# Kernel tuning notes

Hardware: AMD Instinct MI355X
Metric: run time of the kernel (lower is better)

## Reference

```python
import jax, jax.numpy as jnp
import numpy as np

D_MODEL = 768
D_INNER = 1536
D_STATE = 16
D_CONV = 4
DT_RANK = 48
BATCH = 1
SEQ = 2048


def setup_inputs() -> dict:
    key = jax.random.key(0)
    ks = jax.random.split(key, 8)
    s = 0.02
    x = jax.random.normal(ks[0], (BATCH, SEQ, D_MODEL), dtype=jnp.float32)
    W_in = jax.random.normal(ks[1], (2 * D_INNER, D_MODEL), dtype=jnp.float32) * s
    conv_w = jax.random.normal(ks[2], (D_INNER, 1, D_CONV), dtype=jnp.float32) * s
    conv_b = jnp.zeros((D_INNER,), dtype=jnp.float32)
    W_x = jax.random.normal(ks[3], (DT_RANK + 2 * D_STATE, D_INNER), dtype=jnp.float32) * s
    W_dt = jax.random.normal(ks[4], (D_INNER, DT_RANK), dtype=jnp.float32) * s
    b_dt = jax.random.normal(ks[5], (D_INNER,), dtype=jnp.float32) * s
    # A = arange(1, d_state+1) broadcast over d_inner; parameter is log(A)
    A_log = jnp.log(jnp.broadcast_to(jnp.arange(1, D_STATE + 1, dtype=jnp.float32), (D_INNER, D_STATE)))
    D_param = jnp.ones((D_INNER,), dtype=jnp.float32)
    W_out = jax.random.normal(ks[6], (D_MODEL, D_INNER), dtype=jnp.float32) * s
    return {"x": x, "W_in": W_in, "conv_w": conv_w, "conv_b": conv_b, "W_x": W_x,
            "W_dt": W_dt, "b_dt": b_dt, "A_log": A_log, "D_param": D_param, "W_out": W_out}


def _mamba_forward(x, W_in, conv_w, conv_b, W_x, W_dt, b_dt, A_log, D_param, W_out):
    B, L, _ = x.shape
    # in_proj and split into conv branch and gate
    xz = x @ W_in.T                              # [B, L, 2*d_inner]
    xb, z = jnp.split(xz, 2, axis=-1)
    # causal depthwise conv1d (padding=d_conv-1 then trim == left pad d_conv-1)
    xc = jnp.transpose(xb, (0, 2, 1))            # [B, d_inner, L]
    xc = jax.lax.conv_general_dilated(
        xc, conv_w, window_strides=(1,), padding=[(D_CONV - 1, 0)],
        feature_group_count=D_INNER, dimension_numbers=("NCH", "OIH", "NCH"))
    xc = xc + conv_b[None, :, None]
    xb = jax.nn.silu(jnp.transpose(xc, (0, 2, 1)))  # [B, L, d_inner]
    # input-dependent dt, B, C
    xdbl = xb @ W_x.T                            # [B, L, dt_rank + 2*d_state]
    dt = xdbl[..., :DT_RANK]
    Bm = xdbl[..., DT_RANK:DT_RANK + D_STATE]
    Cm = xdbl[..., DT_RANK + D_STATE:]
    dt = jax.nn.softplus(dt @ W_dt.T + b_dt)     # [B, L, d_inner]
    # discretize
    A = -jnp.exp(A_log)                          # [d_inner, d_state]
    dA = jnp.exp(jnp.einsum("bld,dn->bldn", dt, A))          # [B, L, d_inner, d_state]
    dBx = dt[..., None] * Bm[:, :, None, :] * xb[..., None]   # dB * x, [B, L, d_inner, d_state]
    # sequential scan: h[t] = dA[t]*h[t-1] + dBx[t]; y[t] = <h[t], C[t]>
    def step(h, inp):
        dA_t, dBx_t, C_t = inp
        h = dA_t * h + dBx_t                     # [B, d_inner, d_state]
        y_t = jnp.einsum("bdn,bn->bd", h, C_t)
        return h, y_t
    h0 = jnp.zeros((B, D_INNER, D_STATE), dtype=x.dtype)
    _, ys = jax.lax.scan(step, h0, (jnp.moveaxis(dA, 1, 0), jnp.moveaxis(dBx, 1, 0), jnp.moveaxis(Cm, 1, 0)))
    y = jnp.moveaxis(ys, 0, 1) + xb * D_param    # [B, L, d_inner]
    # gate and output projection
    y = y * jax.nn.silu(z)
    return y @ W_out.T                           # [B, L, d_model]


def reference(x, W_in, conv_w, conv_b, W_x, W_dt, b_dt, A_log, D_param, W_out):
    return _mamba_forward(x, W_in, conv_w, conv_b, W_x, W_dt, b_dt, A_log, D_param, W_out)
```

## Files before the change

kernel.cpp:

```cpp
#include <hip/hip_runtime.h>
#include <hip/hip_bf16.h>

#define D_MODEL 768
#define D_INNER 1536
#define D_STATE 16
#define DT_RANK 48
#define SEQ 2048
#define NC 32
#define LC (SEQ / NC)
#define DN (D_INNER * D_STATE)
#define KS 8
#define KCH (D_INNER / KS)

typedef float f32x4 __attribute__((ext_vector_type(4)));
typedef short bf16x8 __attribute__((ext_vector_type(8)));

typedef const __attribute__((address_space(1))) unsigned int* gas_u32;
typedef __attribute__((address_space(3))) unsigned int* las_u32;

__device__ __forceinline__ void gload16(const void* g, void* l) {
  __builtin_amdgcn_global_load_lds((gas_u32)g, (las_u32)l, 16, 0, 0);
}

__device__ __forceinline__ float dpp_radd16(float v) {
  int x;
  x = __builtin_amdgcn_update_dpp(0, __float_as_int(v), 0xB1, 0xF, 0xF, true);
  v += __int_as_float(x);
  x = __builtin_amdgcn_update_dpp(0, __float_as_int(v), 0x4E, 0xF, 0xF, true);
  v += __int_as_float(x);
  x = __builtin_amdgcn_update_dpp(0, __float_as_int(v), 0x141, 0xF, 0xF, true);
  v += __int_as_float(x);
  x = __builtin_amdgcn_update_dpp(0, __float_as_int(v), 0x140, 0xF, 0xF, true);
  v += __int_as_float(x);
  return v;
}

__device__ __forceinline__ ushort f2bf_bits(float f) {
  uint u = __float_as_uint(f);
  u += 0x7FFFu + ((u >> 16) & 1u);
  return (ushort)(u >> 16);
}
__device__ __forceinline__ float bf_bits2f(ushort b) {
  return __uint_as_float(((uint)b) << 16);
}

__device__ __forceinline__ void split_vec4(const float* __restrict__ src,
                                           ushort* __restrict__ hi,
                                           ushort* __restrict__ lo, int idx) {
  const float4 v = ((const float4*)src)[idx];
  const float f[4] = {v.x, v.y, v.z, v.w};
  ushort4 h, l;
  ushort* hp = (ushort*)&h;
  ushort* lp = (ushort*)&l;
#pragma unroll
  for (int j = 0; j < 4; ++j) {
    const ushort hb = f2bf_bits(f[j]);
    hp[j] = hb;
    lp[j] = f2bf_bits(f[j] - bf_bits2f(hb));
  }
  ((ushort4*)hi)[idx] = h;
  ((ushort4*)lo)[idx] = l;
}

__global__ __launch_bounds__(256) void split3_bf16_kernel(
    const float* __restrict__ s0, ushort* __restrict__ h0, ushort* __restrict__ l0, int n0v,
    const float* __restrict__ s1, ushort* __restrict__ h1, ushort* __restrict__ l1, int n1v,
    const float* __restrict__ s2, ushort* __restrict__ h2, ushort* __restrict__ l2) {
  int idx = blockIdx.x * 256 + threadIdx.x;
  if (idx < n0v) {
    split_vec4(s0, h0, l0, idx);
  } else if (idx < n0v + n1v) {
    split_vec4(s1, h1, l1, idx - n0v);
  } else {
    split_vec4(s2, h2, l2, idx - n0v - n1v);
  }
}

template <int BM, int BN>
__global__ __launch_bounds__(256) void gemm_mfma_presplit(
    const ushort* __restrict__ Ah, const ushort* __restrict__ Al, int lda,
    const ushort* __restrict__ Bh, const ushort* __restrict__ Bl, int ldb,
    float* __restrict__ C, int ldc, int K) {
  __shared__ __align__(16) ushort As_hi[BM * 64];
  __shared__ __align__(16) ushort As_lo[BM * 64];
  __shared__ __align__(16) ushort Bs_hi[BN * 64];
  __shared__ __align__(16) ushort Bs_lo[BN * 64];

  const int tid = threadIdx.x;
  const int lane = tid & 63;
  const int wave = tid >> 6;
  const int wbase = tid & 192;
  const int m0 = blockIdx.y * BM;
  const int n0 = blockIdx.x * BN;

  constexpr int FM = BM / 32;
  constexpr int FN = BN / 32;
  const int wm0 = (wave >> 1) * (BM / 2);
  const int wn0 = (wave & 1) * (BN / 2);
  const int fr = lane & 15;
  const int kg = lane >> 4;

  f32x4 acc[FM][FN] = {};

  for (int k0 = 0; k0 < K; k0 += 64) {
#pragma unroll
    for (int i = 0; i < BM / 32; ++i) {
      const int slot = i * 256 + tid;
      const int row = slot >> 3;
      const int c8 = ((slot & 7) ^ (row & 7)) << 3;
      const size_t g = (size_t)(m0 + row) * lda + k0 + c8;
      const int lb = (i * 256 + wbase) * 8;
      gload16(&Ah[g], &As_hi[lb]);
      gload16(&Al[g], &As_lo[lb]);
    }
#pragma unroll
    for (int i = 0; i < BN / 32; ++i) {
      const int slot = i * 256 + tid;
      const int row = slot >> 3;
      const int c8 = ((slot & 7) ^ (row & 7)) << 3;
      const size_t g = (size_t)(n0 + row) * ldb + k0 + c8;
      const int lb = (i * 256 + wbase) * 8;
      gload16(&Bh[g], &Bs_hi[lb]);
      gload16(&Bl[g], &Bs_lo[lb]);
    }
    __syncthreads();

#pragma unroll
    for (int k2 = 0; k2 < 64; k2 += 32) {
      const int gslot = (k2 >> 3) + kg;
      bf16x8 ah[FM], al[FM];
#pragma unroll
      for (int m = 0; m < FM; ++m) {
        const int row = wm0 + m * 16 + fr;
        const int base = row * 64 + ((gslot ^ (row & 7)) << 3);
        ah[m] = *(const bf16x8*)&As_hi[base];
        al[m] = *(const bf16x8*)&As_lo[base];
      }
#pragma unroll
      for (int n = 0; n < FN; ++n) {
        const int row = wn0 + n * 16 + fr;
        const int base = row * 64 + ((gslot ^ (row & 7)) << 3);
        const bf16x8 bh = *(const bf16x8*)&Bs_hi[base];
        const bf16x8 bl = *(const bf16x8*)&Bs_lo[base];
#pragma unroll
        for (int m = 0; m < FM; ++m) {
          acc[m][n] = __builtin_amdgcn_mfma_f32_16x16x32_bf16(ah[m], bh, acc[m][n], 0, 0, 0);
          acc[m][n] = __builtin_amdgcn_mfma_f32_16x16x32_bf16(ah[m], bl, acc[m][n], 0, 0, 0);
          acc[m][n] = __builtin_amdgcn_mfma_f32_16x16x32_bf16(al[m], bh, acc[m][n], 0, 0, 0);
        }
      }
    }
    __syncthreads();
  }

#pragma unroll
  for (int m = 0; m < FM; ++m) {
#pragma unroll
    for (int n = 0; n < FN; ++n) {
      const int row = m0 + wm0 + m * 16 + (lane >> 4) * 4;
      const int col = n0 + wn0 + n * 16 + (lane & 15);
#pragma unroll
      for (int r = 0; r < 4; ++r) C[(row + r) * ldc + col] = acc[m][n][r];
    }
  }
}

__global__ __launch_bounds__(256) void gemm2_splitk(
    const float* __restrict__ A,
    const float* __restrict__ B,
    float* __restrict__ part) {
  __shared__ __align__(16) float As[16][68];
  __shared__ __align__(16) float Bs[16][84];

  const int tid = threadIdx.x;
  const int tx = tid & 15;
  const int ty = tid >> 4;
  const int m0 = blockIdx.x * 64;
  const int kbase = blockIdx.y * KCH;

  float acc[4][5] = {};

  for (int k0 = 0; k0 < KCH; k0 += 16) {
    {
      const int am = tid >> 2;
      const int ak = (tid & 3) << 2;
      const float4 av = *(const float4*)&A[(m0 + am) * D_INNER + kbase + k0 + ak];
      As[ak + 0][am] = av.x;
      As[ak + 1][am] = av.y;
      As[ak + 2][am] = av.z;
      As[ak + 3][am] = av.w;
    }
    for (int f = tid; f < 80 * 4; f += 256) {
      const int row = f >> 2;
      const int kk = (f & 3) << 2;
      const float4 bv = *(const float4*)&B[row * D_INNER + kbase + k0 + kk];
      Bs[kk + 0][row] = bv.x;
      Bs[kk + 1][row] = bv.y;
      Bs[kk + 2][row] = bv.z;
      Bs[kk + 3][row] = bv.w;
    }
    __syncthreads();

#pragma unroll
    for (int k = 0; k < 16; ++k) {
      const float4 a4 = *(const float4*)&As[k][ty * 4];
      const float a[4] = {a4.x, a4.y, a4.z, a4.w};
      float b[5];
#pragma unroll
      for (int j = 0; j < 5; ++j) b[j] = Bs[k][tx + 16 * j];
#pragma unroll
      for (int i = 0; i < 4; ++i)
#pragma unroll
        for (int j = 0; j < 5; ++j) acc[i][j] = fmaf(a[i], b[j], acc[i][j]);
    }
    __syncthreads();
  }

  const int pb = (blockIdx.y * SEQ + m0) * 80;
#pragma unroll
  for (int i = 0; i < 4; ++i)
#pragma unroll
    for (int j = 0; j < 5; ++j)
      part[pb + (ty * 4 + i) * 80 + tx + 16 * j] = acc[i][j];
}

__global__ __launch_bounds__(256) void gemm2_reduce(
    const float* __restrict__ part, float* __restrict__ xdbl) {
  const int idx = blockIdx.x * 256 + threadIdx.x;
  float s = 0.f;
#pragma unroll
  for (int ks = 0; ks < KS; ++ks) s += part[ks * SEQ * 80 + idx];
  xdbl[idx] = s;
}

template <int MODE>
__global__ __launch_bounds__(256) void gemm_kernel(
    const float* __restrict__ A, int lda,
    const float* __restrict__ B, int ldb,
    const float* __restrict__ bias,
    float* __restrict__ C, int ldc,
    int M, int N, int K) {
  __shared__ __align__(16) float As[16][68];
  __shared__ __align__(16) float Bs[16][68];

  const int tid = threadIdx.x;
  const int tx = tid & 15;
  const int ty = tid >> 4;
  const int m0 = blockIdx.y * 64;
  const int n0 = blockIdx.x * 64;

  const int am = tid >> 2;
  const int ak = (tid & 3) << 2;

  float acc[4][4] = {};

  for (int k0 = 0; k0 < K; k0 += 16) {
    {
      const float4 av = *(const float4*)&A[(m0 + am) * lda + k0 + ak];
      As[ak + 0][am] = av.x;
      As[ak + 1][am] = av.y;
      As[ak + 2][am] = av.z;
      As[ak + 3][am] = av.w;
    }
    {
      const int bn = n0 + am;
      float4 bv = make_float4(0.f, 0.f, 0.f, 0.f);
      if (bn < N) bv = *(const float4*)&B[bn * ldb + k0 + ak];
      Bs[ak + 0][am] = bv.x;
      Bs[ak + 1][am] = bv.y;
      Bs[ak + 2][am] = bv.z;
      Bs[ak + 3][am] = bv.w;
    }
    __syncthreads();

#pragma unroll
    for (int k = 0; k < 16; ++k) {
      const float4 a = *(const float4*)&As[k][ty * 4];
      const float4 b = *(const float4*)&Bs[k][tx * 4];
      const float ar[4] = {a.x, a.y, a.z, a.w};
      const float br[4] = {b.x, b.y, b.z, b.w};
#pragma unroll
      for (int i = 0; i < 4; ++i)
#pragma unroll
        for (int j = 0; j < 4; ++j) acc[i][j] = fmaf(ar[i], br[j], acc[i][j]);
    }
    __syncthreads();
  }

#pragma unroll
  for (int i = 0; i < 4; ++i) {
    const int m = m0 + ty * 4 + i;
#pragma unroll
    for (int j = 0; j < 4; ++j) {
      const int n = n0 + tx * 4 + j;
      if (n < N) {
        float v = acc[i][j];
        if (MODE == 1) {
          v += bias[n];
          v = (v > 20.f) ? v : log1pf(__expf(v));
        }
        C[m * ldc + n] = v;
      }
    }
  }
}

__global__ __launch_bounds__(256) void conv_silu_kernel(
    const float* __restrict__ xz, const float* __restrict__ cw,
    const float* __restrict__ cb, float* __restrict__ xbc) {
  const int idx = blockIdx.x * 256 + threadIdx.x;
  const int t = idx / (D_INNER / 4);
  const int d = (idx - t * (D_INNER / 4)) * 4;
  const float4 w0 = *(const float4*)&cw[(d + 0) * 4];
  const float4 w1 = *(const float4*)&cw[(d + 1) * 4];
  const float4 w2 = *(const float4*)&cw[(d + 2) * 4];
  const float4 w3 = *(const float4*)&cw[(d + 3) * 4];
  float4 acc = *(const float4*)&cb[d];
#pragma unroll
  for (int j = 0; j < 4; ++j) {
    const int tt = t + j - 3;
    if (tt >= 0) {
      const float4 xv = *(const float4*)&xz[tt * (2 * D_INNER) + d];
      acc.x = fmaf(xv.x, ((const float*)&w0)[j], acc.x);
      acc.y = fmaf(xv.y, ((const float*)&w1)[j], acc.y);
      acc.z = fmaf(xv.z, ((const float*)&w2)[j], acc.z);
      acc.w = fmaf(xv.w, ((const float*)&w3)[j], acc.w);
    }
  }
  float4 r;
  r.x = acc.x / (1.f + __expf(-acc.x));
  r.y = acc.y / (1.f + __expf(-acc.y));
  r.z = acc.z / (1.f + __expf(-acc.z));
  r.w = acc.w / (1.f + __expf(-acc.w));
  *(float4*)&xbc[t * D_INNER + d] = r;
}

__global__ __launch_bounds__(256) void scan_part1(
    const float* __restrict__ dt, const float* __restrict__ xdbl,
    const float* __restrict__ xbc, const float* __restrict__ A_log,
    float* __restrict__ aprod, float* __restrict__ hloc) {
  __shared__ __align__(16) float dt_s[16][68];
  __shared__ __align__(16) float xb_s[16][68];
  __shared__ __align__(16) float B_s[16][68];

  const int tid = threadIdx.x;
  const int ch = tid >> 4;
  const int n = tid & 15;
  const int d0 = blockIdx.x * 16;
  const int c = blockIdx.y;
  const int t0 = c * LC;

  const float alog = A_log[(d0 + ch) * D_STATE + n];

  for (int f = tid; f < LC * 16; f += 256) {
    const int t = f >> 4, cc = f & 15;
    const int gt = t0 + t;
    dt_s[cc][t] = dt[gt * D_INNER + d0 + cc];
    xb_s[cc][t] = xbc[gt * D_INNER + d0 + cc];
    B_s[cc][t] = xdbl[gt * 80 + DT_RANK + cc];
  }
  __syncthreads();

  const float Aval = -__expf(alog);
  float h = 0.f, ap = 1.f;
  for (int t4 = 0; t4 < LC; t4 += 4) {
    const float4 dtv = *(const float4*)&dt_s[ch][t4];
    const float4 xbv = *(const float4*)&xb_s[ch][t4];
    const float4 Bv = *(const float4*)&B_s[n][t4];
#pragma unroll
    for (int j = 0; j < 4; ++j) {
      const float sdt = ((const float*)&dtv)[j];
      const float dA = __expf(sdt * Aval);
      h = fmaf(dA, h, sdt * ((const float*)&Bv)[j] * ((const float*)&xbv)[j]);
      ap *= dA;
    }
  }
  const int idx = c * DN + d0 * 16 + tid;
  aprod[idx] = ap;
  hloc[idx] = h;
}

__global__ __launch_bounds__(256) void scan_combine(
    const float* __restrict__ aprod, const float* __restrict__ hloc,
    float* __restrict__ hstart) {
  const int idx = blockIdx.x * 256 + threadIdx.x;
  float hs = 0.f;
#pragma unroll
  for (int c = 0; c < NC; ++c) {
    const float a = aprod[c * DN + idx];
    const float hl = hloc[c * DN + idx];
    hstart[c * DN + idx] = hs;
    hs = fmaf(a, hs, hl);
  }
}

__global__ __launch_bounds__(256) void scan_part3(
    const float* __restrict__ dt, const float* __restrict__ xdbl,
    const float* __restrict__ xbc, const float* __restrict__ xz,
    const float* __restrict__ A_log, const float* __restrict__ Dp,
    const float* __restrict__ hstart,
    ushort* __restrict__ ym_hi, ushort* __restrict__ ym_lo) {
  __shared__ __align__(16) float dt_s[16][68];
  __shared__ __align__(16) float xb_s[16][68];
  __shared__ __align__(16) float B_s[16][68];
  __shared__ __align__(16) float C_s[16][68];
  __shared__ float y_s[LC][16];

  const int tid = threadIdx.x;
  const int ch = tid >> 4;
  const int n = tid & 15;
  const int d0 = blockIdx.x * 16;
  const int c = blockIdx.y;
  const int t0 = c * LC;

  float h = hstart[c * DN + d0 * 16 + tid];
  const float alog = A_log[(d0 + ch) * D_STATE + n];
  float zpf[4], dpf[4];
#pragma unroll
  for (int u = 0; u < 4; ++u) {
    const int f = u * 256 + tid;
    const int t = f >> 4, cc = f & 15;
    zpf[u] = xz[(size_t)(t0 + t) * (2 * D_INNER) + D_INNER + d0 + cc];
    dpf[u] = Dp[d0 + cc];
  }

  for (int f = tid; f < LC * 16; f += 256) {
    const int t = f >> 4, cc = f & 15;
    const int gt = t0 + t;
    dt_s[cc][t] = dt[gt * D_INNER + d0 + cc];
    xb_s[cc][t] = xbc[gt * D_INNER + d0 + cc];
    B_s[cc][t] = xdbl[gt * 80 + DT_RANK + cc];
    C_s[cc][t] = xdbl[gt * 80 + DT_RANK + D_STATE + cc];
  }
  __syncthreads();

  const float Aval = -__expf(alog);

  for (int t4 = 0; t4 < LC; t4 += 4) {
    const float4 dtv = *(const float4*)&dt_s[ch][t4];
    const float4 xbv = *(const float4*)&xb_s[ch][t4];
    const float4 Bv = *(const float4*)&B_s[n][t4];
    const float4 Cv = *(const float4*)&C_s[n][t4];
#pragma unroll
    for (int j = 0; j < 4; ++j) {
      const float sdt = ((const float*)&dtv)[j];
      const float dA = __expf(sdt * Aval);
      h = fmaf(dA, h, sdt * ((const float*)&Bv)[j] * ((const float*)&xbv)[j]);
      const float p = dpp_radd16(h * ((const float*)&Cv)[j]);
      if (n == 0) y_s[t4 + j][ch] = p;
    }
  }
  __syncthreads();

#pragma unroll
  for (int u = 0; u < 4; ++u) {
    const int f = u * 256 + tid;
    const int t = f >> 4, cc = f & 15;
    const int gt = t0 + t;
    const float zz = zpf[u];
    const float sig = 1.f / (1.f + __expf(-zz));
    const float v = (y_s[t][cc] + xb_s[cc][t] * dpf[u]) * (zz * sig);
    const ushort hb = f2bf_bits(v);
    const int gidx = gt * D_INNER + d0 + cc;
    ym_hi[gidx] = hb;
    ym_lo[gidx] = f2bf_bits(v - bf_bits2f(hb));
  }
}

extern "C" void kernel_launch(void* const* d_in, const int* in_sizes, int n_in,
                              void* d_out, int out_size, void* d_ws,
                              size_t ws_size, hipStream_t stream) {
  const float* x = (const float*)d_in[0];
  const float* W_in = (const float*)d_in[1];
  const float* conv_w = (const float*)d_in[2];
  const float* conv_b = (const float*)d_in[3];
  const float* W_x = (const float*)d_in[4];
  const float* W_dt = (const float*)d_in[5];
  const float* b_dt = (const float*)d_in[6];
  const float* A_log = (const float*)d_in[7];
  const float* D_param = (const float*)d_in[8];
  const float* W_out = (const float*)d_in[9];
  float* out = (float*)d_out;

  float* ws = (float*)d_ws;
  float* xz = ws;
  float* xbc = xz + SEQ * 2 * D_INNER;
  float* xdbl = xbc + SEQ * D_INNER;
  float* dtb = xdbl + SEQ * 80;
  float* aprod = dtb + SEQ * D_INNER;
  float* hloc = aprod + NC * DN;
  float* hstart = hloc + NC * DN;

  ushort* x_hi = (ushort*)(hstart + NC * DN);
  ushort* x_lo = x_hi + SEQ * D_MODEL;
  ushort* wi_hi = x_lo + SEQ * D_MODEL;
  ushort* wi_lo = wi_hi + 2 * D_INNER * D_MODEL;
  ushort* wo_hi = wi_lo + 2 * D_INNER * D_MODEL;
  ushort* wo_lo = wo_hi + D_MODEL * D_INNER;
  ushort* ym_hi = wo_lo + D_MODEL * D_INNER;
  ushort* ym_lo = ym_hi + SEQ * D_INNER;

  float* part = (float*)x_hi;

  const dim3 blk(256);

  const int n0v = SEQ * D_MODEL / 4;
  const int n1v = 2 * D_INNER * D_MODEL / 4;
  const int n2v = D_MODEL * D_INNER / 4;
  split3_bf16_kernel<<<dim3((n0v + n1v + n2v) / 256), blk, 0, stream>>>(
      x, x_hi, x_lo, n0v, W_in, wi_hi, wi_lo, n1v, W_out, wo_hi, wo_lo);

  gemm_mfma_presplit<128, 64><<<dim3(2 * D_INNER / 64, SEQ / 128), blk, 0, stream>>>(
      x_hi, x_lo, D_MODEL, wi_hi, wi_lo, D_MODEL, xz, 2 * D_INNER, D_MODEL);

  conv_silu_kernel<<<dim3(SEQ * D_INNER / 1024), blk, 0, stream>>>(
      xz, conv_w, conv_b, xbc);

  gemm2_splitk<<<dim3(SEQ / 64, KS), blk, 0, stream>>>(xbc, W_x, part);
  gemm2_reduce<<<dim3(SEQ * 80 / 256), blk, 0, stream>>>(part, xdbl);

  gemm_kernel<1><<<dim3(D_INNER / 64, SEQ / 64), blk, 0, stream>>>(
      xdbl, 80, W_dt, DT_RANK, b_dt, dtb, D_INNER, SEQ, D_INNER, DT_RANK);

  scan_part1<<<dim3(D_INNER / 16, NC), blk, 0, stream>>>(
      dtb, xdbl, xbc, A_log, aprod, hloc);
  scan_combine<<<dim3(DN / 256), blk, 0, stream>>>(aprod, hloc, hstart);
  scan_part3<<<dim3(D_INNER / 16, NC), blk, 0, stream>>>(
      dtb, xdbl, xbc, xz, A_log, D_param, hstart, ym_hi, ym_lo);

  gemm_mfma_presplit<64, 64><<<dim3(D_MODEL / 64, SEQ / 64), blk, 0, stream>>>(
      ym_hi, ym_lo, D_INNER, wo_hi, wo_lo, D_INNER, out, D_MODEL, D_INNER);
}
```

Baseline: 259.7 us.

## Fuse dt projection into scan kernels and use atomic split-K reduction

The dt = softplus(xdbl·W_dtᵀ + b) GEMM is no longer a separate kernel. Each scan block now computes its own 64×16 dt tile in shared memory, so the SEQ×D_INNER dt buffer is never written or read back. The split-K x_proj GEMM accumulates straight into xdbl with relaxed atomics, and conv_silu zeroes xdbl first, which removes the partial buffer and the reduce kernel. In exchange, the dt tile is computed twice (once in scan_part1 and once in scan_part3), floating-point summation order is no longer deterministic, and the scan kernels use more shared memory.

```diff
diff --git a/kernel.cpp b/kernel.cpp
--- a/kernel.cpp
+++ b/kernel.cpp
@@ -168,7 +168,7 @@
 __global__ __launch_bounds__(256) void gemm2_splitk(
     const float* __restrict__ A,
     const float* __restrict__ B,
-    float* __restrict__ part) {
+    float* __restrict__ xdbl) {
   __shared__ __align__(16) float As[16][68];
   __shared__ __align__(16) float Bs[16][84];
 
@@ -216,99 +216,21 @@
     __syncthreads();
   }
 
-  const int pb = (blockIdx.y * SEQ + m0) * 80;
 #pragma unroll
   for (int i = 0; i < 4; ++i)
 #pragma unroll
     for (int j = 0; j < 5; ++j)
-      part[pb + (ty * 4 + i) * 80 + tx + 16 * j] = acc[i][j];
-}
-
-__global__ __launch_bounds__(256) void gemm2_reduce(
-    const float* __restrict__ part, float* __restrict__ xdbl) {
-  const int idx = blockIdx.x * 256 + threadIdx.x;
-  float s = 0.f;
-#pragma unroll
-  for (int ks = 0; ks < KS; ++ks) s += part[ks * SEQ * 80 + idx];
-  xdbl[idx] = s;
-}
-
-template <int MODE>
-__global__ __launch_bounds__(256) void gemm_kernel(
-    const float* __restrict__ A, int lda,
-    const float* __restrict__ B, int ldb,
-    const float* __restrict__ bias,
-    float* __restrict__ C, int ldc,
-    int M, int N, int K) {
-  __shared__ __align__(16) float As[16][68];
-  __shared__ __align__(16) float Bs[16][68];
-
-  const int tid = threadIdx.x;
-  const int tx = tid & 15;
-  const int ty = tid >> 4;
-  const int m0 = blockIdx.y * 64;
-  const int n0 = blockIdx.x * 64;
-
-  const int am = tid >> 2;
-  const int ak = (tid & 3) << 2;
-
-  float acc[4][4] = {};
-
-  for (int k0 = 0; k0 < K; k0 += 16) {
-    {
-      const float4 av = *(const float4*)&A[(m0 + am) * lda + k0 + ak];
-      As[ak + 0][am] = av.x;
-      As[ak + 1][am] = av.y;
-      As[ak + 2][am] = av.z;
-      As[ak + 3][am] = av.w;
-    }
-    {
-      const int bn = n0 + am;
-      float4 bv = make_float4(0.f, 0.f, 0.f, 0.f);
-      if (bn < N) bv = *(const float4*)&B[bn * ldb + k0 + ak];
-      Bs[ak + 0][am] = bv.x;
-      Bs[ak + 1][am] = bv.y;
-      Bs[ak + 2][am] = bv.z;
-      Bs[ak + 3][am] = bv.w;
-    }
-    __syncthreads();
-
-#pragma unroll
-    for (int k = 0; k < 16; ++k) {
-      const float4 a = *(const float4*)&As[k][ty * 4];
-      const float4 b = *(const float4*)&Bs[k][tx * 4];
-      const float ar[4] = {a.x, a.y, a.z, a.w};
-      const float br[4] = {b.x, b.y, b.z, b.w};
-#pragma unroll
-      for (int i = 0; i < 4; ++i)
-#pragma unroll
-        for (int j = 0; j < 4; ++j) acc[i][j] = fmaf(ar[i], br[j], acc[i][j]);
-    }
-    __syncthreads();
-  }
-
-#pragma unroll
-  for (int i = 0; i < 4; ++i) {
-    const int m = m0 + ty * 4 + i;
-#pragma unroll
-    for (int j = 0; j < 4; ++j) {
-      const int n = n0 + tx * 4 + j;
-      if (n < N) {
-        float v = acc[i][j];
-        if (MODE == 1) {
-          v += bias[n];
-          v = (v > 20.f) ? v : log1pf(__expf(v));
-        }
-        C[m * ldc + n] = v;
-      }
-    }
-  }
+      __hip_atomic_fetch_add(&xdbl[(m0 + ty * 4 + i) * 80 + tx + 16 * j],
+                             acc[i][j], __ATOMIC_RELAXED,
+                             __HIP_MEMORY_SCOPE_AGENT);
 }
 
 __global__ __launch_bounds__(256) void conv_silu_kernel(
     const float* __restrict__ xz, const float* __restrict__ cw,
-    const float* __restrict__ cb, float* __restrict__ xbc) {
+    const float* __restrict__ cb, float* __restrict__ xbc,
+    float* __restrict__ xdbl) {
   const int idx = blockIdx.x * 256 + threadIdx.x;
+  if (blockIdx.x < 640) xdbl[blockIdx.x * 256 + threadIdx.x] = 0.f;
   const int t = idx / (D_INNER / 4);
   const int d = (idx - t * (D_INNER / 4)) * 4;
   const float4 w0 = *(const float4*)&cw[(d + 0) * 4];
@@ -335,13 +257,60 @@
   *(float4*)&xbc[t * D_INNER + d] = r;
 }
 
+__device__ __forceinline__ void compute_dt_tile(
+    const float* __restrict__ xdbl, const float* __restrict__ W_dt,
+    const float* __restrict__ b_dt, int t0, int d0, int tid,
+    float* __restrict__ uni, float (*dt_s)[68]) {
+  float (*xd)[52] = (float(*)[52])uni;
+  float* wdt = uni + 64 * 52;
+  float* bd = wdt + 16 * 48;
+#pragma unroll
+  for (int i = 0; i < 3; ++i) {
+    const int s = i * 256 + tid;
+    const int row = s / 12;
+    const int c4 = (s - row * 12) * 4;
+    *(float4*)&xd[row][c4] = *(const float4*)&xdbl[(t0 + row) * 80 + c4];
+  }
+  if (tid < 192) {
+    const int row = tid / 12;
+    const int c4 = (tid - row * 12) * 4;
+    *(float4*)&wdt[row * 48 + c4] = *(const float4*)&W_dt[(d0 + row) * 48 + c4];
+  } else if (tid < 208) {
+    bd[tid - 192] = b_dt[d0 + tid - 192];
+  }
+  __syncthreads();
+
+  const int ch = tid >> 4, tg = tid & 15;
+  float4 w[12];
+#pragma unroll
+  for (int i = 0; i < 12; ++i) w[i] = *(const float4*)&wdt[ch * 48 + i * 4];
+  const float bias = bd[ch];
+#pragma unroll
+  for (int j = 0; j < 4; ++j) {
+    const int t = tg + 16 * j;
+    float acc = 0.f;
+#pragma unroll
+    for (int i = 0; i < 12; ++i) {
+      const float4 xv = *(const float4*)&xd[t][i * 4];
+      acc = fmaf(xv.x, w[i].x, acc);
+      acc = fmaf(xv.y, w[i].y, acc);
+      acc = fmaf(xv.z, w[i].z, acc);
+      acc = fmaf(xv.w, w[i].w, acc);
+    }
+    acc += bias;
+    dt_s[ch][t] = (acc > 20.f) ? acc : log1pf(__expf(acc));
+  }
+  __syncthreads();
+}
+
 __global__ __launch_bounds__(256) void scan_part1(
-    const float* __restrict__ dt, const float* __restrict__ xdbl,
-    const float* __restrict__ xbc, const float* __restrict__ A_log,
+    const float* __restrict__ xdbl, const float* __restrict__ xbc,
+    const float* __restrict__ W_dt, const float* __restrict__ b_dt,
+    const float* __restrict__ A_log,
     float* __restrict__ aprod, float* __restrict__ hloc) {
-  __shared__ __align__(16) float dt_s[16][68];
-  __shared__ __align__(16) float xb_s[16][68];
-  __shared__ __align__(16) float B_s[16][68];
+  __shared__ __align__(16) float smem[16 * 68 + 4112];
+  float (*dt_s)[68] = (float(*)[68])smem;
+  float* uni = smem + 16 * 68;
 
   const int tid = threadIdx.x;
   const int ch = tid >> 4;
@@ -352,10 +321,13 @@
 
   const float alog = A_log[(d0 + ch) * D_STATE + n];
 
+  compute_dt_tile(xdbl, W_dt, b_dt, t0, d0, tid, uni, dt_s);
+
+  float (*xb_s)[68] = (float(*)[68])uni;
+  float (*B_s)[68] = (float(*)[68])(uni + 16 * 68);
   for (int f = tid; f < LC * 16; f += 256) {
     const int t = f >> 4, cc = f & 15;
     const int gt = t0 + t;
-    dt_s[cc][t] = dt[gt * D_INNER + d0 + cc];
     xb_s[cc][t] = xbc[gt * D_INNER + d0 + cc];
     B_s[cc][t] = xdbl[gt * 80 + DT_RANK + cc];
   }
@@ -395,16 +367,15 @@
 }
 
 __global__ __launch_bounds__(256) void scan_part3(
-    const float* __restrict__ dt, const float* __restrict__ xdbl,
-    const float* __restrict__ xbc, const float* __restrict__ xz,
-    const float* __restrict__ A_log, const float* __restrict__ Dp,
-    const float* __restrict__ hstart,
+    const float* __restrict__ xdbl, const float* __restrict__ xbc,
+    const float* __restrict__ xz, const float* __restrict__ W_dt,
+    const float* __restrict__ b_dt, const float* __restrict__ A_log,
+    const float* __restrict__ Dp, const float* __restrict__ hstart,
     ushort* __restrict__ ym_hi, ushort* __restrict__ ym_lo) {
-  __shared__ __align__(16) float dt_s[16][68];
-  __shared__ __align__(16) float xb_s[16][68];
-  __shared__ __align__(16) float B_s[16][68];
-  __shared__ __align__(16) float C_s[16][68];
-  __shared__ float y_s[LC][16];
+  __shared__ __align__(16) float smem[16 * 68 + LC * 16 + 4112];
+  float (*dt_s)[68] = (float(*)[68])smem;
+  float (*y_s)[16] = (float(*)[16])(smem + 16 * 68);
+  float* uni = smem + 16 * 68 + LC * 16;
 
   const int tid = threadIdx.x;
   const int ch = tid >> 4;
@@ -424,10 +395,14 @@
     dpf[u] = Dp[d0 + cc];
   }
 
+  compute_dt_tile(xdbl, W_dt, b_dt, t0, d0, tid, uni, dt_s);
+
+  float (*xb_s)[68] = (float(*)[68])uni;
+  float (*B_s)[68] = (float(*)[68])(uni + 16 * 68);
+  float (*C_s)[68] = (float(*)[68])(uni + 32 * 68);
   for (int f = tid; f < LC * 16; f += 256) {
     const int t = f >> 4, cc = f & 15;
     const int gt = t0 + t;
-    dt_s[cc][t] = dt[gt * D_INNER + d0 + cc];
     xb_s[cc][t] = xbc[gt * D_INNER + d0 + cc];
     B_s[cc][t] = xdbl[gt * 80 + DT_RANK + cc];
     C_s[cc][t] = xdbl[gt * 80 + DT_RANK + D_STATE + cc];
@@ -486,8 +461,7 @@
   float* xz = ws;
   float* xbc = xz + SEQ * 2 * D_INNER;
   float* xdbl = xbc + SEQ * D_INNER;
-  float* dtb = xdbl + SEQ * 80;
-  float* aprod = dtb + SEQ * D_INNER;
+  float* aprod = xdbl + SEQ * 80;
   float* hloc = aprod + NC * DN;
   float* hstart = hloc + NC * DN;
 
@@ -500,8 +474,6 @@
   ushort* ym_hi = wo_lo + D_MODEL * D_INNER;
   ushort* ym_lo = ym_hi + SEQ * D_INNER;
 
-  float* part = (float*)x_hi;
-
   const dim3 blk(256);
 
   const int n0v = SEQ * D_MODEL / 4;
@@ -514,19 +486,15 @@
       x_hi, x_lo, D_MODEL, wi_hi, wi_lo, D_MODEL, xz, 2 * D_INNER, D_MODEL);
 
   conv_silu_kernel<<<dim3(SEQ * D_INNER / 1024), blk, 0, stream>>>(
-      xz, conv_w, conv_b, xbc);
-
-  gemm2_splitk<<<dim3(SEQ / 64, KS), blk, 0, stream>>>(xbc, W_x, part);
-  gemm2_reduce<<<dim3(SEQ * 80 / 256), blk, 0, stream>>>(part, xdbl);
-
-  gemm_kernel<1><<<dim3(D_INNER / 64, SEQ / 64), blk, 0, stream>>>(
-      xdbl, 80, W_dt, DT_RANK, b_dt, dtb, D_INNER, SEQ, D_INNER, DT_RANK);
+      xz, conv_w, conv_b, xbc, xdbl);
+
+  gemm2_splitk<<<dim3(SEQ / 64, KS), blk, 0, stream>>>(xbc, W_x, xdbl);
 
   scan_part1<<<dim3(D_INNER / 16, NC), blk, 0, stream>>>(
-      dtb, xdbl, xbc, A_log, aprod, hloc);
+      xdbl, xbc, W_dt, b_dt, A_log, aprod, hloc);
   scan_combine<<<dim3(DN / 256), blk, 0, stream>>>(aprod, hloc, hstart);
   scan_part3<<<dim3(D_INNER / 16, NC), blk, 0, stream>>>(
-      dtb, xdbl, xbc, xz, A_log, D_param, hstart, ym_hi, ym_lo);
+      xdbl, xbc, xz, W_dt, b_dt, A_log, D_param, hstart, ym_hi, ym_lo);
 
   gemm_mfma_presplit<64, 64><<<dim3(D_MODEL / 64, SEQ / 64), blk, 0, stream>>>(
       ym_hi, ym_lo, D_INNER, wo_hi, wo_lo, D_INNER, out, D_MODEL, D_INNER);
```

New measurement: 264.8 us. No clear change (+2.0%).
